# Kernel tuning notes

Measured on AMD Instinct MI355X. Metric: run time of the kernel, lower is better.

The kernel has to match this reference:

```python
import jax, jax.numpy as jnp
import numpy as np

B, D_IN, D_OUT = 64, 1024, 1024

def setup_inputs() -> dict:
    key = jax.random.key(0)
    ks = jax.random.split(key, 7)
    return {
        "a_mean": jax.random.normal(ks[0], (B, D_IN), jnp.float32),
        "a_cov": jax.random.normal(ks[1], (B, D_IN, D_IN), jnp.float32),
        "weight": jax.random.normal(ks[2], (D_OUT, D_IN), jnp.float32) / np.sqrt(D_IN),
        "bias": jax.random.normal(ks[3], (D_OUT,), jnp.float32),
        "w_kfacs_A": jax.random.normal(ks[4], (D_IN, D_IN), jnp.float32) / np.sqrt(D_IN),
        "w_kfacs_B": jax.random.normal(ks[5], (D_OUT, D_OUT), jnp.float32) / np.sqrt(D_OUT),
        "b_cov": jax.random.normal(ks[6], (D_OUT, D_OUT), jnp.float32),
    }

def reference(a_mean, a_cov, weight, bias, w_kfacs_A, w_kfacs_B, b_cov):
    # h_mean = a_mean @ W^T + b
    h_mean = a_mean @ weight.T + bias  # [B, D_out]
    # Kron term: einsum('ni,nj,kl,ij->nkl') = (a_mean_n^T A a_mean_n) * B_kl
    s = jnp.einsum('ni,ij,nj->n', a_mean, w_kfacs_A, a_mean)  # [B]
    # Trace term: einsum('nij,kl,ij->nkl') = (sum_ij a_cov_nij * A_ij) * B_kl
    t = jnp.einsum('nij,ij->n', a_cov, w_kfacs_A)  # [B]
    kron_term = (s + t)[:, None, None] * w_kfacs_B  # [B, D_out, D_out]
    # Input-cov term: W @ a_cov_n @ W^T
    wcov = jnp.einsum('ki,nij,lj->nkl', weight, a_cov, weight)  # [B, D_out, D_out]
    h_cov = kron_term + wcov + b_cov
    return (h_mean, h_cov)
```

## Files before the change

### kernel.cpp

```cpp
#include <hip/hip_runtime.h>
#include <hip/hip_bf16.h>

typedef short bf16x8 __attribute__((ext_vector_type(8)));
typedef float f32x4  __attribute__((ext_vector_type(4)));

#define KD 1024

__device__ __forceinline__ short f2bf(float f) {
  unsigned u = __builtin_bit_cast(unsigned, f);
  u += 0x7fffu + ((u >> 16) & 1u);
  return (short)(u >> 16);
}

__device__ __forceinline__ void gll16(const short* g, short* l) {
  __builtin_amdgcn_global_load_lds((const __attribute__((address_space(1))) unsigned int*)g,
                                   (__attribute__((address_space(3))) unsigned int*)l,
                                   16, 0, 0);
}

template <int MODE>
__global__ __launch_bounds__(256) void gemm_bt(
    const short* __restrict__ A, size_t a_bs,
    const short* __restrict__ B, size_t b_bs,
    float* __restrict__ out, size_t o_bs,
    short* __restrict__ tout, size_t t_bs,
    const float* __restrict__ kB, const float* __restrict__ bcv,
    const float* __restrict__ cvec, int ncv0,
    const float* __restrict__ bias, int M) {
  __shared__ short sA[128 * 32];
  __shared__ short sB[128 * 32];
  const int t = threadIdx.x;
  const int z = blockIdx.z;
  const short* Ab = A + (size_t)z * a_bs;
  const short* Bb = B + (size_t)z * b_bs;
  const int m0 = blockIdx.y * 128, n0 = blockIdx.x * 128;
  const int lane = t & 63, wv = t >> 6;
  const int wm = (wv >> 1) * 64, wn = (wv & 1) * 64;
  const int r16 = lane & 15, q = lane >> 4;

  const int srow = wv * 16 + (lane >> 2);
  const int skof = (lane & 3) * 8;
  short* lA0 = &sA[(wv * 16) * 32];
  short* lA1 = &sA[(64 + wv * 16) * 32];
  short* lB0 = &sB[(wv * 16) * 32];
  short* lB1 = &sB[(64 + wv * 16) * 32];
  const int ar0 = min(m0 + srow, M - 1);
  const int ar1 = min(m0 + 64 + srow, M - 1);
  const short* gA0 = Ab + (size_t)ar0 * KD + skof;
  const short* gA1 = Ab + (size_t)ar1 * KD + skof;
  const short* gB0 = Bb + (size_t)(n0 + srow) * KD + skof;
  const short* gB1 = Bb + (size_t)(n0 + 64 + srow) * KD + skof;

  f32x4 acc[4][4];
  const f32x4 zero4 = {0.f, 0.f, 0.f, 0.f};
#pragma unroll
  for (int i = 0; i < 4; ++i)
#pragma unroll
    for (int j = 0; j < 4; ++j) acc[i][j] = zero4;

  for (int k0 = 0; k0 < KD; k0 += 32) {
    __syncthreads();
    gll16(gA0 + k0, lA0);
    gll16(gA1 + k0, lA1);
    gll16(gB0 + k0, lB0);
    gll16(gB1 + k0, lB1);
    __syncthreads();

    bf16x8 af[4], bf[4];
#pragma unroll
    for (int i = 0; i < 4; ++i) {
      af[i] = *(const bf16x8*)&sA[(wm + i * 16 + r16) * 32 + q * 8];
      bf[i] = *(const bf16x8*)&sB[(wn + i * 16 + r16) * 32 + q * 8];
    }
#pragma unroll
    for (int mi = 0; mi < 4; ++mi)
#pragma unroll
      for (int ni = 0; ni < 4; ++ni)
        acc[mi][ni] = __builtin_amdgcn_mfma_f32_16x16x32_bf16(af[mi], bf[ni], acc[mi][ni], 0, 0, 0);
  }

  float cv = 0.f;
  if (MODE == 2) cv = cvec[ncv0 + z];
  float* ob = out ? out + (size_t)z * o_bs : nullptr;

#pragma unroll
  for (int mi = 0; mi < 4; ++mi) {
#pragma unroll
    for (int ni = 0; ni < 4; ++ni) {
      const int row0 = m0 + wm + mi * 16 + q * 4;
      const int col = n0 + wn + ni * 16 + r16;
      f32x4 a = acc[mi][ni];
      if (MODE == 0) {
        float bv = bias[col];
#pragma unroll
        for (int r = 0; r < 4; ++r)
          if (row0 + r < M) ob[(size_t)(row0 + r) * 1024 + col] = a[r] + bv;
      } else if (MODE == 1) {
        short4 s;
        s.x = f2bf(a[0]); s.y = f2bf(a[1]); s.z = f2bf(a[2]); s.w = f2bf(a[3]);
        *(short4*)(tout + (size_t)z * t_bs + (size_t)col * 1024 + row0) = s;
      } else {
#pragma unroll
        for (int r = 0; r < 4; ++r) {
          size_t idx = (size_t)(row0 + r) * 1024 + col;
          ob[idx] = a[r] + cv * kB[idx] + bcv[idx];
        }
      }
    }
  }
}

template <int MODE>
__global__ __launch_bounds__(512, 2) void gemm256(
    const short* __restrict__ A, size_t a_bs,
    const short* __restrict__ B, size_t b_bs,
    float* __restrict__ out, size_t o_bs,
    short* __restrict__ tout, size_t t_bs,
    const float* __restrict__ kB, const float* __restrict__ bcv,
    const float* __restrict__ cvec, int ncv0) {
  extern __shared__ short lds[];
  short* ldsB = lds + 32768;
  const int t = threadIdx.x;
  const int z = blockIdx.z;
  const short* Ab = A + (size_t)z * a_bs;
  const short* Bb = B + (size_t)z * b_bs;
  const int m0 = blockIdx.y * 256, n0 = blockIdx.x * 256;
  const int lane = t & 63, wv = t >> 6;
  const int wm = (wv >> 2) * 128, wn = (wv & 3) * 64;
  const int r16 = lane & 15, q = lane >> 4;
  const int sw0 = ((q ^ (r16 & 7)) << 3);
  const int sw1 = (((4 + q) ^ (r16 & 7)) << 3);

  const int trow = t >> 3;
  const int scol = (((t & 7) ^ (trow & 7)) << 3);
  const short* gAa = Ab + (size_t)(m0 + trow) * KD + scol;
  const short* gBa = Bb + (size_t)(n0 + trow) * KD + scol;
  short* lAw = lds + wv * 512;
  short* lBw = ldsB + wv * 512;

#define STAGE_A(KT, H) { _Pragma("unroll") for (int r2 = 0; r2 < 2; ++r2) { \
    const int rr = (H) * 2 + r2; \
    gll16(gAa + (size_t)rr * (64 * KD) + (KT) * 64, lAw + ((KT) & 1) * 16384 + rr * 4096); } }
#define STAGE_B(KT, H) { _Pragma("unroll") for (int r2 = 0; r2 < 2; ++r2) { \
    const int rr = (H) * 2 + r2; \
    gll16(gBa + (size_t)rr * (64 * KD) + (KT) * 64, lBw + ((KT) & 1) * 16384 + rr * 4096); } }

  f32x4 acc[8][4];
#pragma unroll
  for (int i = 0; i < 8; ++i)
#pragma unroll
    for (int j = 0; j < 4; ++j) acc[i][j] = (f32x4){0.f, 0.f, 0.f, 0.f};

  STAGE_A(0, 0); STAGE_A(0, 1); STAGE_B(0, 0); STAGE_B(0, 1);
  STAGE_A(1, 0); STAGE_A(1, 1); STAGE_B(1, 0); STAGE_B(1, 1);
  asm volatile("s_waitcnt vmcnt(8)" ::: "memory");
  __builtin_amdgcn_s_barrier();

  bf16x8 af[4][2];
  bf16x8 bb[4][2];

#define READ_A(MH) { _Pragma("unroll") for (int mq = 0; mq < 4; ++mq) { \
    const short* p = sAc + (wm + (MH) * 64 + mq * 16 + r16) * 64; \
    af[mq][0] = *(const bf16x8*)(p + sw0); \
    af[mq][1] = *(const bf16x8*)(p + sw1); } }
#define READ_B(NH) { _Pragma("unroll") for (int nq = 0; nq < 2; ++nq) { \
    const short* p = sBc + (wn + (NH) * 32 + nq * 16 + r16) * 64; \
    bb[(NH) * 2 + nq][0] = *(const bf16x8*)(p + sw0); \
    bb[(NH) * 2 + nq][1] = *(const bf16x8*)(p + sw1); } }
#define MFMA_Q(MH, NH) { _Pragma("unroll") for (int mq = 0; mq < 4; ++mq) \
    _Pragma("unroll") for (int nq = 0; nq < 2; ++nq) { \
      f32x4 c = acc[(MH) * 4 + mq][(NH) * 2 + nq]; \
      c = __builtin_amdgcn_mfma_f32_16x16x32_bf16(af[mq][0], bb[(NH) * 2 + nq][0], c, 0, 0, 0); \
      c = __builtin_amdgcn_mfma_f32_16x16x32_bf16(af[mq][1], bb[(NH) * 2 + nq][1], c, 0, 0, 0); \
      acc[(MH) * 4 + mq][(NH) * 2 + nq] = c; } }
#define BAR_IN() { asm volatile("" ::: "memory"); __builtin_amdgcn_s_barrier(); \
    asm volatile("s_waitcnt lgkmcnt(0)" ::: "memory"); \
    __builtin_amdgcn_sched_barrier(0); __builtin_amdgcn_s_setprio(1); }
#define BAR_OUT() { __builtin_amdgcn_s_setprio(0); asm volatile("" ::: "memory"); \
    __builtin_amdgcn_s_barrier(); }

  for (int g = 0; g < 16; ++g) {
    const short* sAc = lds + (g & 1) * 16384;
    const short* sBc = ldsB + (g & 1) * 16384;
    READ_A(0); READ_B(0);
    BAR_IN(); MFMA_Q(0, 0); BAR_OUT();
    READ_B(1);
    BAR_IN(); MFMA_Q(0, 1); BAR_OUT();
    READ_A(1);
    if (g <= 13) { STAGE_B(g + 2, 0); STAGE_B(g + 2, 1); }
    BAR_IN(); MFMA_Q(1, 0); BAR_OUT();
    if (g <= 13) { STAGE_A(g + 2, 0); STAGE_A(g + 2, 1); }
    asm volatile("" ::: "memory");
    __builtin_amdgcn_s_barrier();
    __builtin_amdgcn_s_setprio(1);
    MFMA_Q(1, 1);
    __builtin_amdgcn_s_setprio(0);
    asm volatile("" ::: "memory");
    if (g <= 13) { asm volatile("s_waitcnt vmcnt(8)" ::: "memory"); }
    else         { asm volatile("s_waitcnt vmcnt(0)" ::: "memory"); }
    __builtin_amdgcn_s_barrier();
  }
#undef STAGE_A
#undef STAGE_B
#undef READ_A
#undef READ_B
#undef MFMA_Q
#undef BAR_IN
#undef BAR_OUT

  float cv = 0.f;
  if (MODE == 2) cv = cvec[ncv0 + z];
  float* ob = out ? out + (size_t)z * o_bs : nullptr;

#pragma unroll
  for (int me = 0; me < 8; ++me) {
#pragma unroll
    for (int ne = 0; ne < 4; ++ne) {
      const int row0 = m0 + wm + me * 16 + q * 4;
      const int col = n0 + wn + ne * 16 + r16;
      f32x4 a = acc[me][ne];
      if (MODE == 1) {
        short4 s;
        s.x = f2bf(a[0]); s.y = f2bf(a[1]); s.z = f2bf(a[2]); s.w = f2bf(a[3]);
        *(short4*)(tout + (size_t)z * t_bs + (size_t)col * 1024 + row0) = s;
      } else {
#pragma unroll
        for (int r = 0; r < 4; ++r) {
          size_t idx = (size_t)(row0 + r) * 1024 + col;
          ob[idx] = a[r] + cv * kB[idx] + bcv[idx];
        }
      }
    }
  }
}

__global__ __launch_bounds__(256) void conv_acov(const float* __restrict__ a_cov,
                                                 const float* __restrict__ a_mean,
                                                 const float* __restrict__ kA,
                                                 short* __restrict__ abf,
                                                 float* __restrict__ c) {
  const int n = blockIdx.x, ch = blockIdx.y, t = threadIdx.x;
  __shared__ float sm[1024];
  for (int j = t; j < 1024; j += 256) sm[j] = a_mean[n * 1024 + j];
  __syncthreads();
  const float4 amv = ((const float4*)sm)[t];
  const size_t cb = ((size_t)n << 20);
  float acc = 0.f;
  for (int i = ch * 64; i < ch * 64 + 64; ++i) {
    float4 Av = ((const float4*)(kA + ((size_t)i << 10)))[t];
    float4 Cv = ((const float4*)(a_cov + cb + ((size_t)i << 10)))[t];
    short4 s;
    s.x = f2bf(Cv.x); s.y = f2bf(Cv.y); s.z = f2bf(Cv.z); s.w = f2bf(Cv.w);
    *(short4*)(abf + cb + ((size_t)i << 10) + t * 4) = s;
    acc += Av.x * Cv.x + Av.y * Cv.y + Av.z * Cv.z + Av.w * Cv.w;
    acc += sm[i] * (Av.x * amv.x + Av.y * amv.y + Av.z * amv.z + Av.w * amv.w);
  }
#pragma unroll
  for (int off = 32; off > 0; off >>= 1) acc += __shfl_down(acc, off);
  __shared__ float red[4];
  if ((t & 63) == 0) red[t >> 6] = acc;
  __syncthreads();
  if (t == 0) atomicAdd(&c[n], red[0] + red[1] + red[2] + red[3]);
}

__global__ __launch_bounds__(256) void convf(const float* __restrict__ src,
                                             short* __restrict__ dst, int n4) {
  int i = blockIdx.x * 256 + threadIdx.x;
  if (i < n4) {
    float4 v = ((const float4*)src)[i];
    short4 s;
    s.x = f2bf(v.x); s.y = f2bf(v.y); s.z = f2bf(v.z); s.w = f2bf(v.w);
    ((short4*)dst)[i] = s;
  }
}

extern "C" void kernel_launch(void* const* d_in, const int* in_sizes, int n_in,
                              void* d_out, int out_size, void* d_ws, size_t ws_size,
                              hipStream_t stream) {
  const float* a_mean = (const float*)d_in[0];
  const float* a_cov  = (const float*)d_in[1];
  const float* weight = (const float*)d_in[2];
  const float* bias   = (const float*)d_in[3];
  const float* kA     = (const float*)d_in[4];
  const float* kB     = (const float*)d_in[5];
  const float* b_cov  = (const float*)d_in[6];
  float* h_mean = (float*)d_out;
  float* h_cov  = h_mean + (size_t)64 * 1024;

  const size_t SLICE = (size_t)1 << 20;
  float* cvec = (float*)d_ws;
  short* Wbf  = (short*)((char*)d_ws + 4096);
  short* ambf = Wbf + SLICE;
  char*  p    = (char*)(ambf + 65536);
  const size_t need_big = (size_t)((char*)p - (char*)d_ws) + 4 * SLICE * 64;
  const bool big = ws_size >= need_big;

  short* abf, *Tt;
  if (big) {
    abf = (short*)p;
    Tt  = abf + 64 * SLICE;
  } else {
    abf = (short*)h_cov;
    Tt  = (short*)(h_cov + 64 * SLICE / 2);
  }

  static int use256 = -1;
  if (use256 < 0) {
    auto k1 = gemm256<1>;
    auto k2 = gemm256<2>;
    bool ok1 = hipFuncSetAttribute(reinterpret_cast<const void*>(k1),
                                   hipFuncAttributeMaxDynamicSharedMemorySize, 131072) == hipSuccess;
    bool ok2 = hipFuncSetAttribute(reinterpret_cast<const void*>(k2),
                                   hipFuncAttributeMaxDynamicSharedMemorySize, 131072) == hipSuccess;
    use256 = (ok1 && ok2) ? 1 : 0;
  }

  hipMemsetAsync(cvec, 0, 64 * sizeof(float), stream);
  convf<<<dim3(1024), 256, 0, stream>>>(weight, Wbf, 262144);
  convf<<<dim3(64), 256, 0, stream>>>(a_mean, ambf, 16384);
  conv_acov<<<dim3(64, 16), 256, 0, stream>>>(a_cov, a_mean, kA, abf, cvec);

  if (use256) {
    gemm256<1><<<dim3(4, 4, 64), 512, 131072, stream>>>(
        abf, SLICE, Wbf, 0, nullptr, 0, Tt, SLICE,
        nullptr, nullptr, nullptr, 0);
  } else {
    gemm_bt<1><<<dim3(8, 8, 64), 256, 0, stream>>>(
        abf, SLICE, Wbf, 0, nullptr, 0, Tt, SLICE,
        nullptr, nullptr, nullptr, 0, nullptr, 1024);
  }

  gemm_bt<0><<<dim3(8, 1, 1), 256, 0, stream>>>(
      ambf, 0, Wbf, 0, h_mean, 0, nullptr, 0,
      nullptr, nullptr, nullptr, 0, bias, 64);

  if (big) {
    if (use256) {
      gemm256<2><<<dim3(4, 4, 64), 512, 131072, stream>>>(
          Wbf, 0, Tt, SLICE, h_cov, SLICE, nullptr, 0,
          kB, b_cov, cvec, 0);
    } else {
      gemm_bt<2><<<dim3(8, 8, 64), 256, 0, stream>>>(
          Wbf, 0, Tt, SLICE, h_cov, SLICE, nullptr, 0,
          kB, b_cov, cvec, 0, nullptr, 1024);
    }
  } else {
    short* T63 = ambf + 65536;
    hipMemcpyAsync(T63, Tt + 63 * SLICE, SLICE * 2, hipMemcpyDeviceToDevice, stream);
    const int st[6] = {0, 32, 48, 56, 60, 62};
    const int ln[6] = {32, 16, 8, 4, 2, 1};
    for (int w = 0; w < 6; ++w) {
      if (use256) {
        gemm256<2><<<dim3(4, 4, ln[w]), 512, 131072, stream>>>(
            Wbf, 0, Tt + (size_t)st[w] * SLICE, SLICE,
            h_cov + (size_t)st[w] * SLICE, SLICE, nullptr, 0,
            kB, b_cov, cvec, st[w]);
      } else {
        gemm_bt<2><<<dim3(8, 8, ln[w]), 256, 0, stream>>>(
            Wbf, 0, Tt + (size_t)st[w] * SLICE, SLICE,
            h_cov + (size_t)st[w] * SLICE, SLICE, nullptr, 0,
            kB, b_cov, cvec, st[w], nullptr, 1024);
      }
    }
    if (use256) {
      gemm256<2><<<dim3(4, 4, 1), 512, 131072, stream>>>(
          Wbf, 0, T63, 0, h_cov + (size_t)63 * SLICE, 0, nullptr, 0,
          kB, b_cov, cvec, 63);
    } else {
      gemm_bt<2><<<dim3(8, 8, 1), 256, 0, stream>>>(
          Wbf, 0, T63, 0, h_cov + (size_t)63 * SLICE, 0, nullptr, 0,
          kB, b_cov, cvec, 63, nullptr, 1024);
    }
  }
}
```

Baseline: 835.7 us.

## Software-pipeline LDS fragment reads with double-buffered registers and fewer barriers

Restructures the GEMM main loop so LDS fragment reads for the next quadrant, and for the next k-tile, are issued before the MFMAs of the current quadrant, using separate a0/a1/b0/b1 register sets. This cuts the per-iteration barriers from seven to two and replaces the explicit lgkmcnt waits with sched_barrier fences. The aim is to hide LDS latency behind MFMA work. It raises register pressure and relies on the compiler inserting correct lgkmcnt waits, and the reworked vmcnt accounting could be wrong for the final iterations.

```diff
diff --git a/kernel.cpp b/kernel.cpp
--- a/kernel.cpp
+++ b/kernel.cpp
@@ -138,12 +138,25 @@
   short* lAw = lds + wv * 512;
   short* lBw = ldsB + wv * 512;
 
-#define STAGE_A(KT, H) { _Pragma("unroll") for (int r2 = 0; r2 < 2; ++r2) { \
-    const int rr = (H) * 2 + r2; \
-    gll16(gAa + (size_t)rr * (64 * KD) + (KT) * 64, lAw + ((KT) & 1) * 16384 + rr * 4096); } }
-#define STAGE_B(KT, H) { _Pragma("unroll") for (int r2 = 0; r2 < 2; ++r2) { \
-    const int rr = (H) * 2 + r2; \
-    gll16(gBa + (size_t)rr * (64 * KD) + (KT) * 64, lBw + ((KT) & 1) * 16384 + rr * 4096); } }
+#define STAGE_A(KT) { _Pragma("unroll") for (int rr = 0; rr < 4; ++rr) \
+    gll16(gAa + (size_t)rr * (64 * KD) + (KT) * 64, lAw + ((KT) & 1) * 16384 + rr * 4096); }
+#define STAGE_B(KT) { _Pragma("unroll") for (int rr = 0; rr < 4; ++rr) \
+    gll16(gBa + (size_t)rr * (64 * KD) + (KT) * 64, lBw + ((KT) & 1) * 16384 + rr * 4096); }
+#define RD_A(DST, BASE, MH) { _Pragma("unroll") for (int mq = 0; mq < 4; ++mq) { \
+    const short* p_ = (BASE) + (wm + (MH) * 64 + mq * 16 + r16) * 64; \
+    DST[mq][0] = *(const bf16x8*)(p_ + sw0); \
+    DST[mq][1] = *(const bf16x8*)(p_ + sw1); } }
+#define RD_B(DST, BASE, NH) { _Pragma("unroll") for (int nq = 0; nq < 2; ++nq) { \
+    const short* p_ = (BASE) + (wn + (NH) * 32 + nq * 16 + r16) * 64; \
+    DST[nq][0] = *(const bf16x8*)(p_ + sw0); \
+    DST[nq][1] = *(const bf16x8*)(p_ + sw1); } }
+#define QUAD(MH, NH, AF, BF) { _Pragma("unroll") for (int mq = 0; mq < 4; ++mq) \
+    _Pragma("unroll") for (int nq = 0; nq < 2; ++nq) { \
+      f32x4 c = acc[(MH) * 4 + mq][(NH) * 2 + nq]; \
+      c = __builtin_amdgcn_mfma_f32_16x16x32_bf16(AF[mq][0], BF[nq][0], c, 0, 0, 0); \
+      c = __builtin_amdgcn_mfma_f32_16x16x32_bf16(AF[mq][1], BF[nq][1], c, 0, 0, 0); \
+      acc[(MH) * 4 + mq][(NH) * 2 + nq] = c; } }
+#define SFENCE() __builtin_amdgcn_sched_barrier(0)
 
   f32x4 acc[8][4];
 #pragma unroll
@@ -151,62 +164,53 @@
 #pragma unroll
     for (int j = 0; j < 4; ++j) acc[i][j] = (f32x4){0.f, 0.f, 0.f, 0.f};
 
-  STAGE_A(0, 0); STAGE_A(0, 1); STAGE_B(0, 0); STAGE_B(0, 1);
-  STAGE_A(1, 0); STAGE_A(1, 1); STAGE_B(1, 0); STAGE_B(1, 1);
+  STAGE_A(0); STAGE_B(0);
+  STAGE_A(1); STAGE_B(1);
   asm volatile("s_waitcnt vmcnt(8)" ::: "memory");
   __builtin_amdgcn_s_barrier();
 
-  bf16x8 af[4][2];
-  bf16x8 bb[4][2];
-
-#define READ_A(MH) { _Pragma("unroll") for (int mq = 0; mq < 4; ++mq) { \
-    const short* p = sAc + (wm + (MH) * 64 + mq * 16 + r16) * 64; \
-    af[mq][0] = *(const bf16x8*)(p + sw0); \
-    af[mq][1] = *(const bf16x8*)(p + sw1); } }
-#define READ_B(NH) { _Pragma("unroll") for (int nq = 0; nq < 2; ++nq) { \
-    const short* p = sBc + (wn + (NH) * 32 + nq * 16 + r16) * 64; \
-    bb[(NH) * 2 + nq][0] = *(const bf16x8*)(p + sw0); \
-    bb[(NH) * 2 + nq][1] = *(const bf16x8*)(p + sw1); } }
-#define MFMA_Q(MH, NH) { _Pragma("unroll") for (int mq = 0; mq < 4; ++mq) \
-    _Pragma("unroll") for (int nq = 0; nq < 2; ++nq) { \
-      f32x4 c = acc[(MH) * 4 + mq][(NH) * 2 + nq]; \
-      c = __builtin_amdgcn_mfma_f32_16x16x32_bf16(af[mq][0], bb[(NH) * 2 + nq][0], c, 0, 0, 0); \
-      c = __builtin_amdgcn_mfma_f32_16x16x32_bf16(af[mq][1], bb[(NH) * 2 + nq][1], c, 0, 0, 0); \
-      acc[(MH) * 4 + mq][(NH) * 2 + nq] = c; } }
-#define BAR_IN() { asm volatile("" ::: "memory"); __builtin_amdgcn_s_barrier(); \
-    asm volatile("s_waitcnt lgkmcnt(0)" ::: "memory"); \
-    __builtin_amdgcn_sched_barrier(0); __builtin_amdgcn_s_setprio(1); }
-#define BAR_OUT() { __builtin_amdgcn_s_setprio(0); asm volatile("" ::: "memory"); \
-    __builtin_amdgcn_s_barrier(); }
-
+  bf16x8 a0[4][2], a1[4][2], b0[2][2], b1[2][2];
+  RD_A(a0, lds, 0);
+  RD_B(b0, ldsB, 0);
+
+#pragma unroll 2
   for (int g = 0; g < 16; ++g) {
-    const short* sAc = lds + (g & 1) * 16384;
-    const short* sBc = ldsB + (g & 1) * 16384;
-    READ_A(0); READ_B(0);
-    BAR_IN(); MFMA_Q(0, 0); BAR_OUT();
-    READ_B(1);
-    BAR_IN(); MFMA_Q(0, 1); BAR_OUT();
-    READ_A(1);
-    if (g <= 13) { STAGE_B(g + 2, 0); STAGE_B(g + 2, 1); }
-    BAR_IN(); MFMA_Q(1, 0); BAR_OUT();
-    if (g <= 13) { STAGE_A(g + 2, 0); STAGE_A(g + 2, 1); }
-    asm volatile("" ::: "memory");
+    const short* cA = lds + (g & 1) * 16384;
+    const short* cB = ldsB + (g & 1) * 16384;
+    const short* nA = lds + ((g & 1) ^ 1) * 16384;
+    const short* nB = ldsB + ((g & 1) ^ 1) * 16384;
+
+    RD_B(b1, cB, 1);
+    SFENCE();
+    __builtin_amdgcn_s_setprio(1); QUAD(0, 0, a0, b0); __builtin_amdgcn_s_setprio(0);
+    SFENCE();
+
+    RD_A(a1, cA, 1);
+    SFENCE();
+    __builtin_amdgcn_s_setprio(1); QUAD(0, 1, a0, b1); __builtin_amdgcn_s_setprio(0);
+    SFENCE();
+
     __builtin_amdgcn_s_barrier();
-    __builtin_amdgcn_s_setprio(1);
-    MFMA_Q(1, 1);
-    __builtin_amdgcn_s_setprio(0);
-    asm volatile("" ::: "memory");
-    if (g <= 13) { asm volatile("s_waitcnt vmcnt(8)" ::: "memory"); }
-    else         { asm volatile("s_waitcnt vmcnt(0)" ::: "memory"); }
+    if (g <= 13) STAGE_B(g + 2);
+    SFENCE();
+    __builtin_amdgcn_s_setprio(1); QUAD(1, 0, a1, b0); __builtin_amdgcn_s_setprio(0);
+    SFENCE();
+    if (g <= 13)      { asm volatile("s_waitcnt vmcnt(4)" ::: "memory"); }
+    else if (g == 14) { asm volatile("s_waitcnt vmcnt(0)" ::: "memory"); }
+
     __builtin_amdgcn_s_barrier();
+    if (g <= 14) { RD_A(a0, nA, 0); RD_B(b0, nB, 0); }
+    if (g <= 13) STAGE_A(g + 2);
+    SFENCE();
+    __builtin_amdgcn_s_setprio(1); QUAD(1, 1, a1, b1); __builtin_amdgcn_s_setprio(0);
+    SFENCE();
   }
 #undef STAGE_A
 #undef STAGE_B
-#undef READ_A
-#undef READ_B
-#undef MFMA_Q
-#undef BAR_IN
-#undef BAR_OUT
+#undef RD_A
+#undef RD_B
+#undef QUAD
+#undef SFENCE
 
   float cv = 0.f;
   if (MODE == 2) cv = cvec[ncv0 + z];
```

After: 811.2 us. -2.9%, faster.
